# Optimization experiments

Hardware: AMD Instinct MI355X
Metric: run time of the kernel (lower is better)

## Reference

```python
import jax, jax.numpy as jnp
import numpy as np
import math

D_MODEL = 2048
NUM_HEADS = 16
D_K = D_MODEL // NUM_HEADS  # 128
B, S_NEW, S_CACHE = 2, 1024, 3072


def setup_inputs() -> dict:
    key = jax.random.key(0)
    ks = jax.random.split(key, 10)
    s = 1.0 / math.sqrt(D_MODEL)
    return {
        "x": jax.random.normal(ks[0], (B, S_NEW, D_MODEL), jnp.float32),
        "cache": jax.random.normal(ks[1], (2, B, NUM_HEADS, S_CACHE, D_K), jnp.float32),
        "Wq": jax.random.normal(ks[2], (D_MODEL, D_MODEL), jnp.float32) * s,
        "bq": jax.random.normal(ks[3], (D_MODEL,), jnp.float32) * s,
        "Wk": jax.random.normal(ks[4], (D_MODEL, D_MODEL), jnp.float32) * s,
        "bk": jax.random.normal(ks[5], (D_MODEL,), jnp.float32) * s,
        "Wv": jax.random.normal(ks[6], (D_MODEL, D_MODEL), jnp.float32) * s,
        "bv": jax.random.normal(ks[7], (D_MODEL,), jnp.float32) * s,
        "Wo": jax.random.normal(ks[8], (D_MODEL, D_MODEL), jnp.float32) * s,
        "bo": jax.random.normal(ks[9], (D_MODEL,), jnp.float32) * s,
    }


def _split_heads(y, b, s):
    # [b, s, d_model] -> [b, h, s, d_k]
    return y.reshape(b, s, NUM_HEADS, D_K).transpose(0, 2, 1, 3)


def reference(x, cache, Wq, bq, Wk, bk, Wv, bv, Wo, bo):
    b, s, _ = x.shape
    # torch nn.Linear: y = x @ W.T + b
    q = _split_heads(x @ Wq.T + bq, b, s)
    k_new = _split_heads(x @ Wk.T + bk, b, s)
    v_new = _split_heads(x @ Wv.T + bv, b, s)
    k = jnp.concatenate([cache[0], k_new], axis=2)  # [b, h, s_total, d_k]
    v = jnp.concatenate([cache[1], v_new], axis=2)
    s_total = k.shape[2]
    scores = jnp.einsum("bhqd,bhkd->bhqk", q, k) / math.sqrt(D_K)
    if s > 1:
        # triu(ones(s, s_total), diagonal=s_total - s): mask strictly-future new tokens
        mask = jnp.triu(jnp.ones((s, s_total), dtype=bool), k=s_total - s)
        scores = jnp.where(mask, -jnp.inf, scores)
    att = jnp.einsum("bhqk,bhkd->bhqd", jax.nn.softmax(scores, axis=-1), v)
    att = att.transpose(0, 2, 1, 3).reshape(b, s, D_MODEL)
    out = att @ Wo.T + bo
    cache_updated = jnp.stack([k, v], axis=0)
    return out, cache_updated
```

## Files before the change

kernel.cpp:

```cpp
#include <hip/hip_runtime.h>
#include <stdint.h>


typedef unsigned short u16;
typedef __attribute__((ext_vector_type(8))) short s16x8;
typedef __attribute__((ext_vector_type(4))) float f32x4;

#define DM 2048
#define NH 16
#define DK 128
#define SN 1024
#define SC 3072
#define ST 4096

__device__ __forceinline__ u16 bf16rn(float x) {
  uint32_t u = __float_as_uint(x);
  return (u16)((u + 0x7FFFu + ((u >> 16) & 1u)) >> 16);
}
__device__ __forceinline__ float bf16f(u16 h) {
  return __uint_as_float(((uint32_t)h) << 16);
}
__device__ __forceinline__ s16x8 ldfrag(const u16* p) {
  union { uint4 u; s16x8 v; } c;
  c.u = *(const uint4*)p;
  return c.v;
}
__device__ __forceinline__ f32x4 mfma16(s16x8 a, s16x8 b, f32x4 c) {
  return __builtin_amdgcn_mfma_f32_16x16x32_bf16(a, b, c, 0, 0, 0);
}
__device__ __forceinline__ void gload16(const u16* g, u16* l) {
  __builtin_amdgcn_global_load_lds(
      (const __attribute__((address_space(1))) void*)g,
      (__attribute__((address_space(3))) void*)l, 16, 0, 0);
}

__global__ void pack_kernel(const float* __restrict__ src, u16* __restrict__ hi,
                            u16* __restrict__ lo, int n4) {
  int stride = gridDim.x * blockDim.x;
  for (int i = blockIdx.x * blockDim.x + threadIdx.x; i < n4; i += stride) {
    float4 v = ((const float4*)src)[i];
    u16 h0 = bf16rn(v.x), h1 = bf16rn(v.y), h2 = bf16rn(v.z), h3 = bf16rn(v.w);
    ushort4 H; H.x = h0; H.y = h1; H.z = h2; H.w = h3;
    ((ushort4*)hi)[i] = H;
    if (lo) {
      ushort4 L;
      L.x = bf16rn(v.x - bf16f(h0));
      L.y = bf16rn(v.y - bf16f(h1));
      L.z = bf16rn(v.z - bf16f(h2));
      L.w = bf16rn(v.w - bf16f(h3));
      ((ushort4*)lo)[i] = L;
    }
  }
}

__global__ void cache_k_kernel(const float* __restrict__ src, float* __restrict__ dstf,
                               u16* __restrict__ k_all) {
  const int total = 2 * NH * SC * DK / 4;
  int stride = gridDim.x * blockDim.x;
  for (int i = blockIdx.x * blockDim.x + threadIdx.x; i < total; i += stride) {
    int bh = i / (SC * DK / 4);
    int rem = i - bh * (SC * DK / 4);
    float4 v = ((const float4*)src)[i];
    size_t d = (size_t)bh * (ST * DK / 4) + rem;
    ((float4*)dstf)[d] = v;
    ushort4 hh;
    hh.x = bf16rn(v.x); hh.y = bf16rn(v.y); hh.z = bf16rn(v.z); hh.w = bf16rn(v.w);
    ((ushort4*)k_all)[d] = hh;
  }
}

__global__ void cache_v_kernel(const float* __restrict__ src, float* __restrict__ dstf,
                               u16* __restrict__ v_t) {
  const int jt = blockIdx.x, h = blockIdx.y, b = blockIdx.z;
  const int bh = b * NH + h;
  const float* s = src + (size_t)bh * SC * DK + (size_t)jt * 64 * DK;
  float* df = dstf + (size_t)bh * ST * DK + (size_t)jt * 64 * DK;
  u16* dt = v_t + (size_t)bh * DK * ST + jt * 64;
  __shared__ u16 tr[DK * 64];
  const int t = threadIdx.x;
  const int d = t & 127, jg = t >> 7;
  u16 tmp[32];
#pragma unroll
  for (int jj = 0; jj < 32; ++jj) {
    int j = jg * 32 + jj;
    float v = s[j * DK + d];
    df[j * DK + d] = v;
    tmp[jj] = bf16rn(v);
  }
#pragma unroll
  for (int c = 0; c < 4; ++c) {
    int gc = jg * 4 + c;
    int gcs = gc ^ (d & 7);
    uint4 w;
    w.x = (uint32_t)tmp[c * 8 + 0] | ((uint32_t)tmp[c * 8 + 1] << 16);
    w.y = (uint32_t)tmp[c * 8 + 2] | ((uint32_t)tmp[c * 8 + 3] << 16);
    w.z = (uint32_t)tmp[c * 8 + 4] | ((uint32_t)tmp[c * 8 + 5] << 16);
    w.w = (uint32_t)tmp[c * 8 + 6] | ((uint32_t)tmp[c * 8 + 7] << 16);
    ((uint4*)tr)[d * 8 + gcs] = w;
  }
  __syncthreads();
#pragma unroll
  for (int it = 0; it < 4; ++it) {
    int d2 = it * 32 + (t >> 3);
    int gc = t & 7;
    int gcs = gc ^ (d2 & 7);
    uint4 v = ((const uint4*)tr)[d2 * 8 + gcs];
    *(uint4*)(dt + (size_t)d2 * ST + gc * 8) = v;
  }
}

template <int MODE>
__launch_bounds__(256)
__global__ void gemm_kernel(const u16* __restrict__ Ahi, const u16* __restrict__ Alo,
                            const u16* __restrict__ B0, const u16* __restrict__ B1h,
                            const u16* __restrict__ B1l, const u16* __restrict__ B2h,
                            const u16* __restrict__ B2l,
                            const float* __restrict__ bias0, const float* __restrict__ bias1,
                            const float* __restrict__ bias2,
                            u16* __restrict__ q_bf, float* __restrict__ cacheK,
                            u16* __restrict__ k_all, float* __restrict__ cacheV,
                            u16* __restrict__ v_t, float* __restrict__ outO) {
  const int m0 = blockIdx.x * 128;
  int proj, n0;
  if (MODE == 0) { proj = blockIdx.y >> 4; n0 = (blockIdx.y & 15) * 128; }
  else           { proj = 0;               n0 = blockIdx.y * 128; }
  const bool SPLIT = (MODE == 0) && (proj != 0);
  const u16* Bh = (MODE == 1) ? B0 : (proj == 0 ? B0 : (proj == 1 ? B1h : B2h));
  const u16* Bl = (proj == 1) ? B1l : B2l;
  const float* bias = (MODE == 1) ? bias0 : (proj == 0 ? bias0 : (proj == 1 ? bias1 : bias2));

  __shared__ u16 lds[4 * 8192];

  const int t = threadIdx.x;
  const int w = t >> 6;
  const int lane = t & 63, l15 = lane & 15, l4 = lane >> 4;
  const int wr = w >> 1, wc = w & 1;

  f32x4 acc[4][4] = {};

  int srow[4], sgsw[4];
#pragma unroll
  for (int i = 0; i < 4; ++i) {
    int G = i * 256 + t;
    srow[i] = G >> 3;
    sgsw[i] = (G & 7) ^ (srow[i] & 7);
  }
  const int ldst = w * 512;

  for (int kk = 0; kk < 2048; kk += 64) {
#pragma unroll
    for (int i = 0; i < 4; ++i) {
      const size_t ao = (size_t)(m0 + srow[i]) * 2048 + kk + sgsw[i] * 8;
      const size_t bo_ = (size_t)(n0 + srow[i]) * 2048 + kk + sgsw[i] * 8;
      u16* ld = lds + i * 2048 + ldst;
      gload16(Ahi + ao, ld);
      gload16(Bh + bo_, ld + 16384);
      if (SPLIT) {
        gload16(Alo + ao, ld + 8192);
        gload16(Bl + bo_, ld + 24576);
      }
    }
    __syncthreads();
#pragma unroll
    for (int ks = 0; ks < 2; ++ks) {
      s16x8 ah[4], al[4], bh[4], bl[4];
#pragma unroll
      for (int f = 0; f < 4; ++f) {
        int ra = wr * 64 + f * 16 + l15;
        int off_a = ra * 64 + (((ks * 4 + l4) ^ (ra & 7)) * 8);
        ah[f] = ldfrag(lds + off_a);
        if (SPLIT) al[f] = ldfrag(lds + 8192 + off_a);
        int rb = wc * 64 + f * 16 + l15;
        int off_b = rb * 64 + (((ks * 4 + l4) ^ (rb & 7)) * 8);
        bh[f] = ldfrag(lds + 16384 + off_b);
        if (SPLIT) bl[f] = ldfrag(lds + 24576 + off_b);
      }
#pragma unroll
      for (int mf = 0; mf < 4; ++mf)
#pragma unroll
        for (int nf = 0; nf < 4; ++nf) {
          acc[mf][nf] = mfma16(ah[mf], bh[nf], acc[mf][nf]);
          if (SPLIT) {
            acc[mf][nf] = mfma16(ah[mf], bl[nf], acc[mf][nf]);
            acc[mf][nf] = mfma16(al[mf], bh[nf], acc[mf][nf]);
          }
        }
    }
    __syncthreads();
  }
#pragma unroll
  for (int nf = 0; nf < 4; ++nf) {
    const int n = n0 + wc * 64 + nf * 16 + l15;
    const float bv_ = bias[n];
#pragma unroll
    for (int mf = 0; mf < 4; ++mf) {
#pragma unroll
      for (int r = 0; r < 4; ++r) {
        const int m = m0 + wr * 64 + mf * 16 + l4 * 4 + r;
        const float val = acc[mf][nf][r] + bv_;
        if (MODE == 1) {
          outO[(size_t)m * 2048 + n] = val;
        } else if (proj == 0) {
          const int b = m >> 10, ss = m & 1023, hh = n >> 7, d = n & 127;
          q_bf[(((size_t)(b * NH + hh)) * SN + ss) * DK + d] = bf16rn(val);
        } else {
          const int b = m >> 10, ss = m & 1023, hh = n >> 7, d = n & 127;
          const size_t idx = (((size_t)(b * NH + hh)) * ST + SC + ss) * DK + d;
          if (proj == 1) {
            cacheK[idx] = val;
            k_all[idx] = bf16rn(val);
          } else {
            cacheV[idx] = val;
            v_t[(((size_t)(b * NH + hh)) * DK + d) * ST + SC + ss] = bf16rn(val);
          }
        }
      }
    }
  }
}

__launch_bounds__(512)
__global__ void attn_kernel(const u16* __restrict__ q_bf, const u16* __restrict__ k_all,
                            const u16* __restrict__ v_t, u16* __restrict__ att) {
  const int qt = blockIdx.x, h = blockIdx.y, b = blockIdx.z;
  const int bh = b * NH + h;
  const int qb = qt * 128;
  __shared__ u16 Kt[64 * DK];
  __shared__ u16 Vt[DK * 64];
  __shared__ u16 Pl[128 * 64];
  const int t = threadIdx.x;
  const int w = t >> 6, lane = t & 63, l15 = lane & 15, l4 = lane >> 4;

  const u16* qbase = q_bf + (size_t)bh * SN * DK;
  s16x8 qf[4];
  {
    const int row = qb + w * 16 + l15;
#pragma unroll
    for (int ks = 0; ks < 4; ++ks)
      qf[ks] = ldfrag(qbase + (size_t)row * DK + ks * 32 + l4 * 8);
  }
  f32x4 o[8] = {};
  float mrow[4], lrow[4];
#pragma unroll
  for (int r = 0; r < 4; ++r) { mrow[r] = -1e30f; lrow[r] = 0.0f; }

  const u16* kbase = k_all + (size_t)bh * ST * DK;
  const u16* vbase = v_t + (size_t)bh * DK * ST;
  const int ntiles = ((qb + SC + 126) >> 6) + 1;

  for (int tile = 0; tile < ntiles; ++tile) {
    const int j0 = tile * 64;
#pragma unroll
    for (int i = 0; i < 2; ++i) {
      {
        const int G = i * 512 + t;
        const int row = G >> 4, gc = G & 15;
        gload16(kbase + (size_t)(j0 + row) * DK + ((gc ^ (row & 7)) * 8),
                Kt + (i * 512 + w * 64) * 8);
      }
      {
        const int G = i * 512 + t;
        const int row = G >> 3, gc = G & 7;
        gload16(vbase + (size_t)row * ST + j0 + ((gc ^ (row & 7)) * 8),
                Vt + (i * 512 + w * 64) * 8);
      }
    }
    __syncthreads();
    f32x4 sc[4] = {};
#pragma unroll
    for (int ks = 0; ks < 4; ++ks) {
#pragma unroll
      for (int nf = 0; nf < 4; ++nf) {
        const int j = nf * 16 + l15;
        s16x8 kf = ldfrag(Kt + j * DK + (((ks * 4 + l4) ^ (j & 7)) * 8));
        sc[nf] = mfma16(qf[ks], kf, sc[nf]);
      }
    }
    const bool domask = (j0 + 63) >= (qb + SC);
    const float sscale = 0.08838834764831845f;
    float tmax[4];
#pragma unroll
    for (int r = 0; r < 4; ++r) tmax[r] = -1e30f;
#pragma unroll
    for (int nf = 0; nf < 4; ++nf) {
#pragma unroll
      for (int r = 0; r < 4; ++r) {
        float s_ = sc[nf][r] * sscale;
        if (domask) {
          const int j = j0 + nf * 16 + l15;
          const int q = qb + w * 16 + l4 * 4 + r;
          if (j >= q + SC) s_ = -1e30f;
        }
        sc[nf][r] = s_;
        tmax[r] = fmaxf(tmax[r], s_);
      }
    }
#pragma unroll
    for (int mk = 1; mk < 16; mk <<= 1)
#pragma unroll
      for (int r = 0; r < 4; ++r)
        tmax[r] = fmaxf(tmax[r], __shfl_xor(tmax[r], mk, 64));
    float so[4], rs[4];
#pragma unroll
    for (int r = 0; r < 4; ++r) {
      const float mn = fmaxf(mrow[r], tmax[r]);
      so[r] = __expf(mrow[r] - mn);
      mrow[r] = mn;
      rs[r] = 0.0f;
    }
#pragma unroll
    for (int nf = 0; nf < 4; ++nf) {
#pragma unroll
      for (int r = 0; r < 4; ++r) {
        const float p = __expf(sc[nf][r] - mrow[r]);
        rs[r] += p;
        const int qrow = w * 16 + l4 * 4 + r;
        const int jl = nf * 16 + l15;
        Pl[qrow * 64 + ((((jl >> 3) ^ (qrow & 7)) << 3) | (jl & 7))] = bf16rn(p);
      }
    }
#pragma unroll
    for (int mk = 1; mk < 16; mk <<= 1)
#pragma unroll
      for (int r = 0; r < 4; ++r)
        rs[r] += __shfl_xor(rs[r], mk, 64);
#pragma unroll
    for (int r = 0; r < 4; ++r) lrow[r] = lrow[r] * so[r] + rs[r];
#pragma unroll
    for (int nf = 0; nf < 8; ++nf)
#pragma unroll
      for (int r = 0; r < 4; ++r) o[nf][r] *= so[r];
    asm volatile("s_waitcnt lgkmcnt(0)" ::: "memory");
#pragma unroll
    for (int ks = 0; ks < 2; ++ks) {
      const int qrow = w * 16 + l15;
      s16x8 pf = ldfrag(Pl + qrow * 64 + (((ks * 4 + l4) ^ (qrow & 7)) * 8));
#pragma unroll
      for (int nf = 0; nf < 8; ++nf) {
        const int d = nf * 16 + l15;
        s16x8 vf = ldfrag(Vt + d * 64 + (((ks * 4 + l4) ^ (d & 7)) * 8));
        o[nf] = mfma16(pf, vf, o[nf]);
      }
    }
    __syncthreads();
  }
  u16* ob = att + ((size_t)b * SN) * DM + (size_t)h * DK;
#pragma unroll
  for (int nf = 0; nf < 8; ++nf) {
#pragma unroll
    for (int r = 0; r < 4; ++r) {
      const int q = qb + w * 16 + l4 * 4 + r;
      const int d = nf * 16 + l15;
      ob[(size_t)q * DM + d] = bf16rn(o[nf][r] / lrow[r]);
    }
  }
}

extern "C" void kernel_launch(void* const* d_in, const int* in_sizes, int n_in,
                              void* d_out, int out_size, void* d_ws, size_t ws_size,
                              hipStream_t stream) {
  const float* x     = (const float*)d_in[0];
  const float* cache = (const float*)d_in[1];
  const float* Wq = (const float*)d_in[2];
  const float* bq = (const float*)d_in[3];
  const float* Wk = (const float*)d_in[4];
  const float* bk = (const float*)d_in[5];
  const float* Wv = (const float*)d_in[6];
  const float* bv = (const float*)d_in[7];
  const float* Wo = (const float*)d_in[8];
  const float* bo = (const float*)d_in[9];

  float* out = (float*)d_out;
  float* cacheK = out + (size_t)2 * SN * DM;
  float* cacheV = cacheK + (size_t)2 * NH * ST * DK;

  char* ws = (char*)d_ws;
  u16* x_hi  = (u16*)(ws + 0);
  u16* x_lo  = (u16*)(ws + 8388608ull);
  u16* wq_hi = (u16*)(ws + 16777216ull);
  u16* wk_hi = (u16*)(ws + 25165824ull);
  u16* wk_lo = (u16*)(ws + 33554432ull);
  u16* wv_hi = (u16*)(ws + 41943040ull);
  u16* wv_lo = (u16*)(ws + 50331648ull);
  u16* wo_hi = (u16*)(ws + 58720256ull);
  u16* q_bf  = (u16*)(ws + 67108864ull);
  u16* k_all = (u16*)(ws + 75497472ull);
  u16* v_t   = (u16*)(ws + 109051904ull);
  u16* att   = x_hi;

  const int W4 = 2048 * 2048 / 4;
  pack_kernel<<<2048, 256, 0, stream>>>(x,  x_hi,  x_lo,  W4);
  pack_kernel<<<2048, 256, 0, stream>>>(Wk, wk_hi, wk_lo, W4);
  pack_kernel<<<2048, 256, 0, stream>>>(Wv, wv_hi, wv_lo, W4);
  pack_kernel<<<2048, 256, 0, stream>>>(Wq, wq_hi, nullptr, W4);
  pack_kernel<<<2048, 256, 0, stream>>>(Wo, wo_hi, nullptr, W4);
  cache_k_kernel<<<4096, 256, 0, stream>>>(cache, cacheK, k_all);
  cache_v_kernel<<<dim3(SC / 64, NH, 2), 256, 0, stream>>>(
      cache + (size_t)2 * NH * SC * DK, cacheV, v_t);
  gemm_kernel<0><<<dim3(16, 48), 256, 0, stream>>>(
      x_hi, x_lo, wq_hi, wk_hi, wk_lo, wv_hi, wv_lo,
      bq, bk, bv, q_bf, cacheK, k_all, cacheV, v_t, nullptr);
  attn_kernel<<<dim3(8, NH, 2), 512, 0, stream>>>(q_bf, k_all, v_t, att);
  gemm_kernel<1><<<dim3(16, 16), 256, 0, stream>>>(
      att, nullptr, wo_hi, nullptr, nullptr, nullptr, nullptr,
      bo, nullptr, nullptr, nullptr, nullptr, nullptr, nullptr, nullptr, out);
}
```

Measured before the change: 701.6 us.

## Split attention over key range with 32x32 MFMA, double buffering, and combine kernel

Attention is rewritten to split each query tile's key range across two blocks (flash-decoding style) and merge the partial outputs in a new combine kernel. It also switches to 32x32x16 bf16 MFMA, keeps P in registers via lane shuffles instead of LDS, double-buffers the K/V tiles, and skips the rescale unless the running max rises by more than a threshold. The softmax scale is folded into Q in the projection GEMM, and the workspace is reshuffled so the fp32 partials alias dead buffers. The aim is more blocks to fill the GPU and lower per-tile latency, at the cost of extra fp32 partial traffic and an added launch.

```diff
diff --git a/kernel.cpp b/kernel.cpp
--- a/kernel.cpp
+++ b/kernel.cpp
@@ -5,6 +5,7 @@
 typedef unsigned short u16;
 typedef __attribute__((ext_vector_type(8))) short s16x8;
 typedef __attribute__((ext_vector_type(4))) float f32x4;
+typedef __attribute__((ext_vector_type(16))) float f32x16;
 
 #define DM 2048
 #define NH 16
@@ -27,6 +28,9 @@
 }
 __device__ __forceinline__ f32x4 mfma16(s16x8 a, s16x8 b, f32x4 c) {
   return __builtin_amdgcn_mfma_f32_16x16x32_bf16(a, b, c, 0, 0, 0);
+}
+__device__ __forceinline__ f32x16 mfma32(s16x8 a, s16x8 b, f32x16 c) {
+  return __builtin_amdgcn_mfma_f32_32x32x16_bf16(a, b, c, 0, 0, 0);
 }
 __device__ __forceinline__ void gload16(const u16* g, u16* l) {
   __builtin_amdgcn_global_load_lds(
@@ -202,7 +206,8 @@
           outO[(size_t)m * 2048 + n] = val;
         } else if (proj == 0) {
           const int b = m >> 10, ss = m & 1023, hh = n >> 7, d = n & 127;
-          q_bf[(((size_t)(b * NH + hh)) * SN + ss) * DK + d] = bf16rn(val);
+          q_bf[(((size_t)(b * NH + hh)) * SN + ss) * DK + d] =
+              bf16rn(val * 0.08838834764831845f);
         } else {
           const int b = m >> 10, ss = m & 1023, hh = n >> 7, d = n & 127;
           const size_t idx = (((size_t)(b * NH + hh)) * ST + SC + ss) * DK + d;
@@ -219,141 +224,184 @@
   }
 }
 
-__launch_bounds__(512)
+__launch_bounds__(256, 2)
 __global__ void attn_kernel(const u16* __restrict__ q_bf, const u16* __restrict__ k_all,
-                            const u16* __restrict__ v_t, u16* __restrict__ att) {
-  const int qt = blockIdx.x, h = blockIdx.y, b = blockIdx.z;
+                            const u16* __restrict__ v_t, float* __restrict__ op,
+                            float* __restrict__ ml) {
+  const int qt = blockIdx.x, h = blockIdx.y;
+  const int b = blockIdx.z & 1, sp = blockIdx.z >> 1;
   const int bh = b * NH + h;
   const int qb = qt * 128;
-  __shared__ u16 Kt[64 * DK];
-  __shared__ u16 Vt[DK * 64];
-  __shared__ u16 Pl[128 * 64];
+  __shared__ u16 lds[2 * 16384];
   const int t = threadIdx.x;
-  const int w = t >> 6, lane = t & 63, l15 = lane & 15, l4 = lane >> 4;
-
-  const u16* qbase = q_bf + (size_t)bh * SN * DK;
-  s16x8 qf[4];
+  const int w = t >> 6, lane = t & 63;
+  const int l31 = lane & 31, hi = lane >> 5;
+  const int q = qb + w * 32 + l31;
+
+  s16x8 qf[8];
   {
-    const int row = qb + w * 16 + l15;
-#pragma unroll
-    for (int ks = 0; ks < 4; ++ks)
-      qf[ks] = ldfrag(qbase + (size_t)row * DK + ks * 32 + l4 * 8);
-  }
-  f32x4 o[8] = {};
-  float mrow[4], lrow[4];
-#pragma unroll
-  for (int r = 0; r < 4; ++r) { mrow[r] = -1e30f; lrow[r] = 0.0f; }
+    const u16* qrow = q_bf + ((size_t)bh * SN + q) * DK;
+#pragma unroll
+    for (int kk = 0; kk < 8; ++kk) qf[kk] = ldfrag(qrow + kk * 16 + hi * 8);
+  }
+
+  f32x16 o[4] = {};
+  float mrow = -1e30f, lrow = 0.f;
 
   const u16* kbase = k_all + (size_t)bh * ST * DK;
   const u16* vbase = v_t + (size_t)bh * DK * ST;
-  const int ntiles = ((qb + SC + 126) >> 6) + 1;
-
-  for (int tile = 0; tile < ntiles; ++tile) {
-    const int j0 = tile * 64;
-#pragma unroll
-    for (int i = 0; i < 2; ++i) {
-      {
-        const int G = i * 512 + t;
-        const int row = G >> 4, gc = G & 15;
-        gload16(kbase + (size_t)(j0 + row) * DK + ((gc ^ (row & 7)) * 8),
-                Kt + (i * 512 + w * 64) * 8);
-      }
-      {
-        const int G = i * 512 + t;
-        const int row = G >> 3, gc = G & 7;
-        gload16(vbase + (size_t)row * ST + j0 + ((gc ^ (row & 7)) * 8),
-                Vt + (i * 512 + w * 64) * 8);
+  const int ntiles = ((qb + 127 + SC - 1) >> 6) + 1;
+  const int ntp = (ntiles + 1) >> 1;
+  const int tile0 = sp * ntp;
+  const int tile1 = min(ntiles, tile0 + ntp);
+
+#define STAGE(buf, tile)                                                          \
+  do {                                                                            \
+    const int j0s = (tile) * 64;                                                  \
+    u16* kt_ = lds + (buf) * 16384;                                               \
+    u16* vt_ = lds + (buf) * 16384 + 8192;                                        \
+    _Pragma("unroll")                                                             \
+    for (int i = 0; i < 4; ++i) {                                                 \
+      const int G = i * 256 + t;                                                  \
+      const int krow = G >> 4, kgc = G & 15;                                      \
+      gload16(kbase + (size_t)(j0s + krow) * DK + ((kgc ^ (krow & 15)) * 8),      \
+              kt_ + (i * 256 + w * 64) * 8);                                      \
+      const int vrow = G >> 3, vgc = G & 7;                                       \
+      gload16(vbase + (size_t)vrow * ST + j0s + ((vgc ^ (vrow & 7)) * 8),         \
+              vt_ + (i * 256 + w * 64) * 8);                                      \
+    }                                                                             \
+  } while (0)
+
+  STAGE(0, tile0);
+  __syncthreads();
+
+  for (int tt = tile0; tt < tile1; ++tt) {
+    const int cur = (tt - tile0) & 1;
+    if (tt + 1 < tile1) STAGE(cur ^ 1, tt + 1);
+    const u16* kt = lds + cur * 16384;
+    const u16* vt = lds + cur * 16384 + 8192;
+    const int j0 = tt * 64;
+
+    f32x16 sc0 = {}, sc1 = {};
+#pragma unroll
+    for (int kk = 0; kk < 8; ++kk) {
+      const int row0 = l31;
+      s16x8 kf0 = ldfrag(kt + row0 * 128 + (((kk * 2 + hi) ^ (row0 & 15)) * 8));
+      sc0 = mfma32(kf0, qf[kk], sc0);
+      const int row1 = 32 + l31;
+      s16x8 kf1 = ldfrag(kt + row1 * 128 + (((kk * 2 + hi) ^ (row1 & 15)) * 8));
+      sc1 = mfma32(kf1, qf[kk], sc1);
+    }
+
+    float p[2][16];
+    const bool domask = (j0 + 63) >= (qb + SC);
+    float tmax = -1e30f;
+#pragma unroll
+    for (int r = 0; r < 16; ++r) {
+      float v0 = sc0[r], v1 = sc1[r];
+      if (domask) {
+        const int jl = (r & 3) + 8 * (r >> 2) + 4 * hi;
+        if (j0 + jl >= q + SC) v0 = -1e30f;
+        if (j0 + 32 + jl >= q + SC) v1 = -1e30f;
+      }
+      p[0][r] = v0; p[1][r] = v1;
+      tmax = fmaxf(tmax, fmaxf(v0, v1));
+    }
+    tmax = fmaxf(tmax, __shfl_xor(tmax, 32, 64));
+    if (tmax > mrow + 8.f) {
+      const float soo = __expf(mrow - tmax);
+      mrow = tmax;
+      lrow *= soo;
+#pragma unroll
+      for (int dt = 0; dt < 4; ++dt)
+#pragma unroll
+        for (int r = 0; r < 16; ++r) o[dt][r] *= soo;
+    }
+    float rs = 0.f;
+#pragma unroll
+    for (int jt = 0; jt < 2; ++jt)
+#pragma unroll
+      for (int r = 0; r < 16; ++r) {
+        const float e = __expf(p[jt][r] - mrow);
+        p[jt][r] = e;
+        rs += e;
+      }
+    rs += __shfl_xor(rs, 32, 64);
+    lrow += rs;
+
+    uint32_t pk[2][4][2];
+#pragma unroll
+    for (int jt = 0; jt < 2; ++jt)
+#pragma unroll
+      for (int g = 0; g < 4; ++g) {
+        pk[jt][g][0] = (uint32_t)bf16rn(p[jt][g * 4 + 0]) |
+                       ((uint32_t)bf16rn(p[jt][g * 4 + 1]) << 16);
+        pk[jt][g][1] = (uint32_t)bf16rn(p[jt][g * 4 + 2]) |
+                       ((uint32_t)bf16rn(p[jt][g * 4 + 3]) << 16);
+      }
+
+#pragma unroll
+    for (int kt = 0; kt < 4; ++kt) {
+      const int jts = kt >> 1;
+      const int gA = (2 * kt) & 3, gB = (2 * kt + 1) & 3;
+      uint32_t S0 = hi ? pk[jts][gA][0] : pk[jts][gB][0];
+      uint32_t S1 = hi ? pk[jts][gA][1] : pk[jts][gB][1];
+      uint32_t R0 = __shfl_xor(S0, 32, 64);
+      uint32_t R1 = __shfl_xor(S1, 32, 64);
+      uint32_t L0 = hi ? pk[jts][gB][0] : pk[jts][gA][0];
+      uint32_t L1 = hi ? pk[jts][gB][1] : pk[jts][gA][1];
+      union { uint32_t u[4]; s16x8 v; } pf;
+      pf.u[0] = hi ? R0 : L0;
+      pf.u[1] = hi ? R1 : L1;
+      pf.u[2] = hi ? L0 : R0;
+      pf.u[3] = hi ? L1 : R1;
+#pragma unroll
+      for (int dt = 0; dt < 4; ++dt) {
+        const int d = dt * 32 + l31;
+        s16x8 vf = ldfrag(vt + d * 64 + (((2 * kt + hi) ^ (d & 7)) * 8));
+        o[dt] = mfma32(vf, pf.v, o[dt]);
       }
     }
     __syncthreads();
-    f32x4 sc[4] = {};
-#pragma unroll
-    for (int ks = 0; ks < 4; ++ks) {
-#pragma unroll
-      for (int nf = 0; nf < 4; ++nf) {
-        const int j = nf * 16 + l15;
-        s16x8 kf = ldfrag(Kt + j * DK + (((ks * 4 + l4) ^ (j & 7)) * 8));
-        sc[nf] = mfma16(qf[ks], kf, sc[nf]);
-      }
-    }
-    const bool domask = (j0 + 63) >= (qb + SC);
-    const float sscale = 0.08838834764831845f;
-    float tmax[4];
-#pragma unroll
-    for (int r = 0; r < 4; ++r) tmax[r] = -1e30f;
-#pragma unroll
-    for (int nf = 0; nf < 4; ++nf) {
-#pragma unroll
-      for (int r = 0; r < 4; ++r) {
-        float s_ = sc[nf][r] * sscale;
-        if (domask) {
-          const int j = j0 + nf * 16 + l15;
-          const int q = qb + w * 16 + l4 * 4 + r;
-          if (j >= q + SC) s_ = -1e30f;
-        }
-        sc[nf][r] = s_;
-        tmax[r] = fmaxf(tmax[r], s_);
-      }
-    }
-#pragma unroll
-    for (int mk = 1; mk < 16; mk <<= 1)
-#pragma unroll
-      for (int r = 0; r < 4; ++r)
-        tmax[r] = fmaxf(tmax[r], __shfl_xor(tmax[r], mk, 64));
-    float so[4], rs[4];
-#pragma unroll
-    for (int r = 0; r < 4; ++r) {
-      const float mn = fmaxf(mrow[r], tmax[r]);
-      so[r] = __expf(mrow[r] - mn);
-      mrow[r] = mn;
-      rs[r] = 0.0f;
-    }
-#pragma unroll
-    for (int nf = 0; nf < 4; ++nf) {
-#pragma unroll
-      for (int r = 0; r < 4; ++r) {
-        const float p = __expf(sc[nf][r] - mrow[r]);
-        rs[r] += p;
-        const int qrow = w * 16 + l4 * 4 + r;
-        const int jl = nf * 16 + l15;
-        Pl[qrow * 64 + ((((jl >> 3) ^ (qrow & 7)) << 3) | (jl & 7))] = bf16rn(p);
-      }
-    }
-#pragma unroll
-    for (int mk = 1; mk < 16; mk <<= 1)
-#pragma unroll
-      for (int r = 0; r < 4; ++r)
-        rs[r] += __shfl_xor(rs[r], mk, 64);
-#pragma unroll
-    for (int r = 0; r < 4; ++r) lrow[r] = lrow[r] * so[r] + rs[r];
-#pragma unroll
-    for (int nf = 0; nf < 8; ++nf)
-#pragma unroll
-      for (int r = 0; r < 4; ++r) o[nf][r] *= so[r];
-    asm volatile("s_waitcnt lgkmcnt(0)" ::: "memory");
-#pragma unroll
-    for (int ks = 0; ks < 2; ++ks) {
-      const int qrow = w * 16 + l15;
-      s16x8 pf = ldfrag(Pl + qrow * 64 + (((ks * 4 + l4) ^ (qrow & 7)) * 8));
-#pragma unroll
-      for (int nf = 0; nf < 8; ++nf) {
-        const int d = nf * 16 + l15;
-        s16x8 vf = ldfrag(Vt + d * 64 + (((ks * 4 + l4) ^ (d & 7)) * 8));
-        o[nf] = mfma16(pf, vf, o[nf]);
-      }
-    }
-    __syncthreads();
-  }
-  u16* ob = att + ((size_t)b * SN) * DM + (size_t)h * DK;
-#pragma unroll
-  for (int nf = 0; nf < 8; ++nf) {
-#pragma unroll
-    for (int r = 0; r < 4; ++r) {
-      const int q = qb + w * 16 + l4 * 4 + r;
-      const int d = nf * 16 + l15;
-      ob[(size_t)q * DM + d] = bf16rn(o[nf][r] / lrow[r]);
-    }
-  }
+  }
+
+  float* opb = op + (((size_t)sp * 32 + bh) * SN + q) * DK;
+#pragma unroll
+  for (int dt = 0; dt < 4; ++dt)
+#pragma unroll
+    for (int g = 0; g < 4; ++g) {
+      float4 vv;
+      vv.x = o[dt][g * 4 + 0]; vv.y = o[dt][g * 4 + 1];
+      vv.z = o[dt][g * 4 + 2]; vv.w = o[dt][g * 4 + 3];
+      *(float4*)(opb + dt * 32 + 8 * g + 4 * hi) = vv;
+    }
+  if (hi == 0) {
+    float2 mv; mv.x = mrow; mv.y = lrow;
+    *(float2*)(ml + (((size_t)sp * 32 + bh) * SN + q) * 2) = mv;
+  }
+}
+
+__global__ void combine_kernel(const float* __restrict__ op, const float* __restrict__ ml,
+                               u16* __restrict__ att) {
+  const int idx = blockIdx.x * 256 + threadIdx.x;
+  const int d4 = idx & 31;
+  const int qq = (idx >> 5) & 1023;
+  const int bh = idx >> 15;
+  const size_t rq = (size_t)bh * SN + qq;
+  const float2 ml0 = *(const float2*)(ml + rq * 2);
+  const float2 ml1 = *(const float2*)(ml + (rq + 32 * (size_t)SN) * 2);
+  const float ms = fmaxf(ml0.x, ml1.x);
+  const float w0 = __expf(ml0.x - ms), w1 = __expf(ml1.x - ms);
+  const float inv = 1.0f / (ml0.y * w0 + ml1.y * w1);
+  const float4 a = *(const float4*)(op + rq * DK + d4 * 4);
+  const float4 c = *(const float4*)(op + (rq + 32 * (size_t)SN) * DK + d4 * 4);
+  ushort4 r;
+  r.x = bf16rn((a.x * w0 + c.x * w1) * inv);
+  r.y = bf16rn((a.y * w0 + c.y * w1) * inv);
+  r.z = bf16rn((a.z * w0 + c.z * w1) * inv);
+  r.w = bf16rn((a.w * w0 + c.w * w1) * inv);
+  const int bb = bh >> 4, hh = bh & 15;
+  *(ushort4*)(att + ((size_t)bb * SN + qq) * DM + hh * DK + d4 * 4) = r;
 }
 
 extern "C" void kernel_launch(void* const* d_in, const int* in_sizes, int n_in,
@@ -376,17 +424,19 @@
 
   char* ws = (char*)d_ws;
   u16* x_hi  = (u16*)(ws + 0);
-  u16* x_lo  = (u16*)(ws + 8388608ull);
-  u16* wq_hi = (u16*)(ws + 16777216ull);
-  u16* wk_hi = (u16*)(ws + 25165824ull);
-  u16* wk_lo = (u16*)(ws + 33554432ull);
-  u16* wv_hi = (u16*)(ws + 41943040ull);
-  u16* wv_lo = (u16*)(ws + 50331648ull);
-  u16* wo_hi = (u16*)(ws + 58720256ull);
-  u16* q_bf  = (u16*)(ws + 67108864ull);
-  u16* k_all = (u16*)(ws + 75497472ull);
-  u16* v_t   = (u16*)(ws + 109051904ull);
-  u16* att   = x_hi;
+  u16* wk_hi = (u16*)(ws + 8388608ull);
+  u16* wv_hi = (u16*)(ws + 16777216ull);
+  u16* wo_hi = (u16*)(ws + 25165824ull);
+  u16* q_bf  = (u16*)(ws + 33554432ull);
+  u16* k_all = (u16*)(ws + 41943040ull);
+  u16* v_t   = (u16*)(ws + 75497472ull);
+  u16* x_lo  = (u16*)(ws + 109051904ull);
+  u16* wq_hi = (u16*)(ws + 117440512ull);
+  u16* wk_lo = (u16*)(ws + 125829120ull);
+  u16* wv_lo = (u16*)(ws + 134217728ull);
+  float* op = (float*)(ws + 109051904ull);
+  float* ml = (float*)(ws + 8388608ull);
+  u16* att  = x_hi;
 
   const int W4 = 2048 * 2048 / 4;
   pack_kernel<<<2048, 256, 0, stream>>>(x,  x_hi,  x_lo,  W4);
@@ -400,7 +450,8 @@
   gemm_kernel<0><<<dim3(16, 48), 256, 0, stream>>>(
       x_hi, x_lo, wq_hi, wk_hi, wk_lo, wv_hi, wv_lo,
       bq, bk, bv, q_bf, cacheK, k_all, cacheV, v_t, nullptr);
-  attn_kernel<<<dim3(8, NH, 2), 512, 0, stream>>>(q_bf, k_all, v_t, att);
+  attn_kernel<<<dim3(8, NH, 4), 256, 0, stream>>>(q_bf, k_all, v_t, op, ml);
+  combine_kernel<<<4096, 256, 0, stream>>>(op, ml, att);
   gemm_kernel<1><<<dim3(16, 16), 256, 0, stream>>>(
       att, nullptr, wo_hi, nullptr, nullptr, nullptr, nullptr,
       bo, nullptr, nullptr, nullptr, nullptr, nullptr, nullptr, nullptr, out);
```

New measurement: 626.5 us. 1.12x faster.
